# Performance work log

Hardware: AMD Instinct MI355X
Metric: run time of the kernel (lower is better)

The kernel has to match this reference:

```python
import jax, jax.numpy as jnp
import numpy as np

N_NODES = 50000
N_EDGES = 600000
D_IN = 128
D_HID = 128


def _gcn_layer(x, src, dst, W, b, n):
    # PyG GCNConv: h = x @ W; add self-loops; symmetric normalization
    # out_i = sum_j (d_i^-1/2 d_j^-1/2) h_j + (d_i^-1) h_i + b, with d = deg + 1
    h = x @ W  # [N, F]
    ones = jnp.ones(src.shape[0], dtype=x.dtype)
    deg = jax.ops.segment_sum(ones, dst, num_segments=n) + jnp.asarray(1.0, x.dtype)
    dinv = jax.lax.rsqrt(deg)  # [N]
    coef = dinv[src] * dinv[dst]  # [E]
    msg = h[src] * coef[:, None]  # gather + scale, [E, F]
    agg = jax.ops.segment_sum(msg, dst, num_segments=n)  # scatter-add, [N, F]
    agg = agg + h * (dinv * dinv)[:, None]  # self-loop contribution
    return agg + b


def setup_inputs() -> dict:
    key = jax.random.key(0)
    k1, k2, k3, k4 = jax.random.split(key, 4)
    x = jax.random.normal(k1, (N_NODES, D_IN), dtype=jnp.float32)
    edge_index = jax.random.randint(k2, (2, N_EDGES), 0, N_NODES, dtype=jnp.int32)
    # Glorot-ish init for linear weights
    W1 = jax.random.normal(k3, (D_IN, D_HID), dtype=jnp.float32) / np.sqrt(D_IN)
    W2 = jax.random.normal(k4, (D_HID, D_HID), dtype=jnp.float32) / np.sqrt(D_HID)
    b1 = jnp.zeros((D_HID,), dtype=jnp.float32)
    b2 = jnp.zeros((D_HID,), dtype=jnp.float32)
    return {"x": x, "edge_index": edge_index, "W1": W1, "b1": b1, "W2": W2, "b2": b2}


def reference(x, edge_index, W1, b1, W2, b2):
    src = edge_index[0]
    dst = edge_index[1]
    n = x.shape[0]
    h = _gcn_layer(x, src, dst, W1, b1, n)
    h = jax.nn.relu(h)
    out = _gcn_layer(h, src, dst, W2, b2, n)
    return out
```

## Files before the change

### kernel.cpp

```cpp
#include <hip/hip_runtime.h>
#include <hip/hip_bf16.h>

typedef __attribute__((ext_vector_type(8))) short short8;
typedef __attribute__((ext_vector_type(4))) float floatx4;

#define D 128
#define BCAP 2048
#define CPAD 16

__device__ __forceinline__ unsigned short f2bf(float f) {
    unsigned u = __float_as_uint(f);
    u += 0x7FFFu + ((u >> 16) & 1u);
    return (unsigned short)(u >> 16);
}
__device__ __forceinline__ float bf2f(unsigned short h) {
    return __uint_as_float(((unsigned)h) << 16);
}
__device__ __forceinline__ float bflo(unsigned p) { return __uint_as_float(p << 16); }
__device__ __forceinline__ float bfhi(unsigned p) { return __uint_as_float(p & 0xFFFF0000u); }

__global__ __launch_bounds__(256) void bucket_wconv_kernel(const int* __restrict__ src,
                                                           const int* __restrict__ dst,
                                                           int* __restrict__ bcnt,
                                                           unsigned* __restrict__ bucket, int E,
                                                           const float* __restrict__ W1,
                                                           const float* __restrict__ W2,
                                                           unsigned short* __restrict__ whi1,
                                                           unsigned short* __restrict__ wlo1,
                                                           unsigned short* __restrict__ whi2,
                                                           unsigned short* __restrict__ wlo2,
                                                           int eb4) {
    int b = blockIdx.x;
    if (b >= eb4) {
        int gid = (b - eb4) * 256 + threadIdx.x;
        int which = gid >> 14;
        int tid = gid & 16383;
        const float* W = which ? W2 : W1;
        unsigned short* whi = which ? whi2 : whi1;
        unsigned short* wlo = which ? wlo2 : wlo1;
        int j    = tid & 7;
        int col  = (tid >> 3) & 127;
        int quad = (tid >> 10) & 3;
        int kb   = tid >> 12;
        float wv = W[(kb * 32 + quad * 8 + j) * D + col];
        unsigned u = __float_as_uint(wv);
        unsigned short h = (unsigned short)(u >> 16);
        whi[tid] = h;
        wlo[tid] = f2bf(wv - bf2f(h));
        return;
    }
    int sub = b & 7;
    int t4 = (b * 256 + threadIdx.x) * 4;
    if (t4 + 3 < E) {
        int4 s = *reinterpret_cast<const int4*>(src + t4);
        int4 d = *reinterpret_cast<const int4*>(dst + t4);
        #pragma unroll
        for (int k = 0; k < 4; k++) {
            int dd = (k == 0) ? d.x : (k == 1) ? d.y : (k == 2) ? d.z : d.w;
            int ss = (k == 0) ? s.x : (k == 1) ? s.y : (k == 2) ? s.z : s.w;
            int slot = ((dd >> 8) << 3) | sub;
            int pos = atomicAdd(&bcnt[slot * CPAD], 1);
            if (pos < BCAP)
                bucket[(size_t)slot * BCAP + pos] = ((unsigned)(dd & 255) << 16) | (unsigned)ss;
        }
    } else {
        for (int i = t4; i < E; i++) {
            int dd = dst[i], ss = src[i];
            int slot = ((dd >> 8) << 3) | sub;
            int pos = atomicAdd(&bcnt[slot * CPAD], 1);
            if (pos < BCAP)
                bucket[(size_t)slot * BCAP + pos] = ((unsigned)(dd & 255) << 16) | (unsigned)ss;
        }
    }
}

__device__ __forceinline__ int block_excl_scan256(int v, int* lds, int tid) {
    int lane = tid & 63, wid = tid >> 6;
    int x = v;
    #pragma unroll
    for (int d = 1; d < 64; d <<= 1) {
        int y = __shfl_up(x, d, 64);
        if (lane >= d) x += y;
    }
    if (lane == 63) lds[wid] = x;
    __syncthreads();
    if (tid == 0) {
        int run = 0;
        #pragma unroll
        for (int i = 0; i < 4; i++) { int t2 = lds[i]; lds[i] = run; run += t2; }
    }
    __syncthreads();
    return lds[wid] + x - v;
}

__global__ __launch_bounds__(256) void build_gemm_kernel(const unsigned* __restrict__ bucket,
                                                         const int* __restrict__ bcnt,
                                                         int* __restrict__ row_ptr,
                                                         float* __restrict__ dinv,
                                                         int* __restrict__ esrc, int N, int E,
                                                         const float* __restrict__ A,
                                                         const unsigned short* __restrict__ whi,
                                                         const unsigned short* __restrict__ wlo,
                                                         unsigned short* __restrict__ C, int M,
                                                         int nbuk) {
    __shared__ int lds4[4];
    __shared__ int sbase[256];
    __shared__ int hist[256];
    __shared__ int cur[256];
    int tid = threadIdx.x;
    int b = blockIdx.x;
    if (b < nbuk) {
        int tot = 0;
        if (tid < nbuk) {
            #pragma unroll
            for (int s = 0; s < 8; s++) tot += min(bcnt[(tid * 8 + s) * CPAD], BCAP);
        }
        int ex = block_excl_scan256(tot, lds4, tid);
        sbase[tid] = ex;
        hist[tid] = 0;
        __syncthreads();
        int base = sbase[b];
        for (int sub = 0; sub < 8; sub++) {
            int cnt = min(bcnt[(b * 8 + sub) * CPAD], BCAP);
            const unsigned* bp = bucket + (size_t)(b * 8 + sub) * BCAP;
            for (int i = tid; i < cnt; i += 256)
                atomicAdd(&hist[bp[i] >> 16], 1);
        }
        __syncthreads();
        int h = hist[tid];
        int off = block_excl_scan256(h, lds4, tid);
        cur[tid] = base + off;
        int node = b * 256 + tid;
        if (node < N) {
            row_ptr[node] = base + off;
            dinv[node] = rsqrtf((float)(h + 1));
        }
        if (b == 0 && tid == 0) row_ptr[N] = E;
        __syncthreads();
        for (int sub = 0; sub < 8; sub++) {
            int cnt = min(bcnt[(b * 8 + sub) * CPAD], BCAP);
            const unsigned* bp = bucket + (size_t)(b * 8 + sub) * BCAP;
            for (int i = tid; i < cnt; i += 256) {
                unsigned v = bp[i];
                int p = atomicAdd(&cur[v >> 16], 1);
                esrc[p] = (int)(v & 0xFFFFu);
            }
        }
        return;
    }
    int lane = tid & 63, wid = tid >> 6;
    int quad = lane >> 4, l15 = lane & 15;
    int row0 = (b - nbuk) * 64;
    int n0 = wid * 32;

    short8 bhi[2][4], blo[2][4];
    #pragma unroll
    for (int t = 0; t < 2; t++)
        #pragma unroll
        for (int kb = 0; kb < 4; kb++) {
            size_t base = ((size_t)((kb * 4 + quad) * 128 + (n0 + t * 16 + l15))) * 8;
            bhi[t][kb] = *reinterpret_cast<const short8*>(whi + base);
            blo[t][kb] = *reinterpret_cast<const short8*>(wlo + base);
        }

    #pragma unroll
    for (int rg = 0; rg < 4; rg++) {
        int r0 = row0 + rg * 16;
        int ar = r0 + l15; if (ar > M - 1) ar = M - 1;
        short8 ahi[4], alo[4];
        #pragma unroll
        for (int kb = 0; kb < 4; kb++) {
            const float4* ap = reinterpret_cast<const float4*>(A + (size_t)ar * D + kb * 32 + quad * 8);
            float4 v0 = ap[0], v1 = ap[1];
            float vv[8] = {v0.x, v0.y, v0.z, v0.w, v1.x, v1.y, v1.z, v1.w};
            short8 vh, vl;
            #pragma unroll
            for (int j = 0; j < 8; j++) {
                unsigned u = __float_as_uint(vv[j]);
                unsigned short h = (unsigned short)(u >> 16);
                vh[j] = (short)h;
                vl[j] = (short)f2bf(vv[j] - bf2f(h));
            }
            ahi[kb] = vh;
            alo[kb] = vl;
        }
        floatx4 acc0 = {0.f, 0.f, 0.f, 0.f};
        floatx4 acc1 = {0.f, 0.f, 0.f, 0.f};
        #pragma unroll
        for (int kb = 0; kb < 4; kb++) {
            acc0 = __builtin_amdgcn_mfma_f32_16x16x32_bf16(ahi[kb], bhi[0][kb], acc0, 0, 0, 0);
            acc1 = __builtin_amdgcn_mfma_f32_16x16x32_bf16(ahi[kb], bhi[1][kb], acc1, 0, 0, 0);
            acc0 = __builtin_amdgcn_mfma_f32_16x16x32_bf16(ahi[kb], blo[0][kb], acc0, 0, 0, 0);
            acc1 = __builtin_amdgcn_mfma_f32_16x16x32_bf16(ahi[kb], blo[1][kb], acc1, 0, 0, 0);
            acc0 = __builtin_amdgcn_mfma_f32_16x16x32_bf16(alo[kb], bhi[0][kb], acc0, 0, 0, 0);
            acc1 = __builtin_amdgcn_mfma_f32_16x16x32_bf16(alo[kb], bhi[1][kb], acc1, 0, 0, 0);
        }
        #pragma unroll
        for (int r = 0; r < 4; r++) {
            int orow = r0 + quad * 4 + r;
            if (orow < M) {
                C[(size_t)orow * D + n0 + l15]      = f2bf(acc0[r]);
                C[(size_t)orow * D + n0 + 16 + l15] = f2bf(acc1[r]);
            }
        }
    }
}

__global__ __launch_bounds__(256) void gemm_bf16a_kernel(const unsigned short* __restrict__ A,
                                                         const unsigned short* __restrict__ whi,
                                                         const unsigned short* __restrict__ wlo,
                                                         unsigned short* __restrict__ C, int M) {
    int lane = threadIdx.x & 63, wid = threadIdx.x >> 6;
    int quad = lane >> 4, l15 = lane & 15;
    int row0 = blockIdx.x * 64;
    int n0 = wid * 32;

    short8 bhi[2][4], blo[2][4];
    #pragma unroll
    for (int t = 0; t < 2; t++)
        #pragma unroll
        for (int kb = 0; kb < 4; kb++) {
            size_t base = ((size_t)((kb * 4 + quad) * 128 + (n0 + t * 16 + l15))) * 8;
            bhi[t][kb] = *reinterpret_cast<const short8*>(whi + base);
            blo[t][kb] = *reinterpret_cast<const short8*>(wlo + base);
        }

    #pragma unroll
    for (int rg = 0; rg < 4; rg++) {
        int r0 = row0 + rg * 16;
        int ar = r0 + l15; if (ar > M - 1) ar = M - 1;
        short8 af[4];
        #pragma unroll
        for (int kb = 0; kb < 4; kb++)
            af[kb] = *reinterpret_cast<const short8*>(A + (size_t)ar * D + kb * 32 + quad * 8);
        floatx4 acc0 = {0.f, 0.f, 0.f, 0.f};
        floatx4 acc1 = {0.f, 0.f, 0.f, 0.f};
        #pragma unroll
        for (int kb = 0; kb < 4; kb++) {
            acc0 = __builtin_amdgcn_mfma_f32_16x16x32_bf16(af[kb], bhi[0][kb], acc0, 0, 0, 0);
            acc1 = __builtin_amdgcn_mfma_f32_16x16x32_bf16(af[kb], bhi[1][kb], acc1, 0, 0, 0);
            acc0 = __builtin_amdgcn_mfma_f32_16x16x32_bf16(af[kb], blo[0][kb], acc0, 0, 0, 0);
            acc1 = __builtin_amdgcn_mfma_f32_16x16x32_bf16(af[kb], blo[1][kb], acc1, 0, 0, 0);
        }
        #pragma unroll
        for (int r = 0; r < 4; r++) {
            int orow = r0 + quad * 4 + r;
            if (orow < M) {
                C[(size_t)orow * D + n0 + l15]      = f2bf(acc0[r]);
                C[(size_t)orow * D + n0 + 16 + l15] = f2bf(acc1[r]);
            }
        }
    }
}

__device__ __forceinline__ void agg_qbody(const uint4* __restrict__ H4,
                                          const float* __restrict__ dinv,
                                          const int* __restrict__ row_ptr,
                                          const int* __restrict__ esrc,
                                          const float* __restrict__ bias,
                                          int node, int fl, float* acc) {
    #pragma unroll
    for (int j = 0; j < 8; j++) acc[j] = 0.f;
    int beg = row_ptr[node], end = row_ptr[node + 1];
    int e = beg;
    for (; e + 4 <= end; e += 4) {
        int s0 = esrc[e], s1 = esrc[e + 1], s2 = esrc[e + 2], s3 = esrc[e + 3];
        float c0 = dinv[s0], c1 = dinv[s1], c2 = dinv[s2], c3 = dinv[s3];
        uint4 p0 = H4[(size_t)s0 * 16 + fl];
        uint4 p1 = H4[(size_t)s1 * 16 + fl];
        uint4 p2 = H4[(size_t)s2 * 16 + fl];
        uint4 p3 = H4[(size_t)s3 * 16 + fl];
        acc[0] += c0 * bflo(p0.x) + c1 * bflo(p1.x) + c2 * bflo(p2.x) + c3 * bflo(p3.x);
        acc[1] += c0 * bfhi(p0.x) + c1 * bfhi(p1.x) + c2 * bfhi(p2.x) + c3 * bfhi(p3.x);
        acc[2] += c0 * bflo(p0.y) + c1 * bflo(p1.y) + c2 * bflo(p2.y) + c3 * bflo(p3.y);
        acc[3] += c0 * bfhi(p0.y) + c1 * bfhi(p1.y) + c2 * bfhi(p2.y) + c3 * bfhi(p3.y);
        acc[4] += c0 * bflo(p0.z) + c1 * bflo(p1.z) + c2 * bflo(p2.z) + c3 * bflo(p3.z);
        acc[5] += c0 * bfhi(p0.z) + c1 * bfhi(p1.z) + c2 * bfhi(p2.z) + c3 * bfhi(p3.z);
        acc[6] += c0 * bflo(p0.w) + c1 * bflo(p1.w) + c2 * bflo(p2.w) + c3 * bflo(p3.w);
        acc[7] += c0 * bfhi(p0.w) + c1 * bfhi(p1.w) + c2 * bfhi(p2.w) + c3 * bfhi(p3.w);
    }
    for (; e < end; e++) {
        int s0 = esrc[e];
        float c = dinv[s0];
        uint4 p0 = H4[(size_t)s0 * 16 + fl];
        acc[0] += c * bflo(p0.x); acc[1] += c * bfhi(p0.x);
        acc[2] += c * bflo(p0.y); acc[3] += c * bfhi(p0.y);
        acc[4] += c * bflo(p0.z); acc[5] += c * bfhi(p0.z);
        acc[6] += c * bflo(p0.w); acc[7] += c * bfhi(p0.w);
    }
    float di = dinv[node];
    float dii = di * di;
    uint4 ps = H4[(size_t)node * 16 + fl];
    const float4* b4 = (const float4*)bias;
    float4 bb0 = b4[fl * 2], bb1 = b4[fl * 2 + 1];
    #pragma unroll
    for (int j = 0; j < 8; j++) acc[j] *= di;
    acc[0] += dii * bflo(ps.x) + bb0.x;
    acc[1] += dii * bfhi(ps.x) + bb0.y;
    acc[2] += dii * bflo(ps.y) + bb0.z;
    acc[3] += dii * bfhi(ps.y) + bb0.w;
    acc[4] += dii * bflo(ps.z) + bb1.x;
    acc[5] += dii * bfhi(ps.z) + bb1.y;
    acc[6] += dii * bflo(ps.w) + bb1.z;
    acc[7] += dii * bfhi(ps.w) + bb1.w;
}

__global__ __launch_bounds__(256) void agg_bf16out_kernel(const unsigned short* __restrict__ H,
                                                          const float* __restrict__ dinv,
                                                          const int* __restrict__ row_ptr,
                                                          const int* __restrict__ esrc,
                                                          const float* __restrict__ bias,
                                                          uint4* __restrict__ out, int N) {
    int node = blockIdx.x * 16 + (threadIdx.x >> 4);
    int fl = threadIdx.x & 15;
    if (node >= N) return;
    float acc[8];
    agg_qbody((const uint4*)H, dinv, row_ptr, esrc, bias, node, fl, acc);
    uint4 o;
    o.x = (unsigned)f2bf(fmaxf(acc[0], 0.f)) | ((unsigned)f2bf(fmaxf(acc[1], 0.f)) << 16);
    o.y = (unsigned)f2bf(fmaxf(acc[2], 0.f)) | ((unsigned)f2bf(fmaxf(acc[3], 0.f)) << 16);
    o.z = (unsigned)f2bf(fmaxf(acc[4], 0.f)) | ((unsigned)f2bf(fmaxf(acc[5], 0.f)) << 16);
    o.w = (unsigned)f2bf(fmaxf(acc[6], 0.f)) | ((unsigned)f2bf(fmaxf(acc[7], 0.f)) << 16);
    out[(size_t)node * 16 + fl] = o;
}

__global__ __launch_bounds__(256) void agg_f32out_kernel(const unsigned short* __restrict__ H,
                                                         const float* __restrict__ dinv,
                                                         const int* __restrict__ row_ptr,
                                                         const int* __restrict__ esrc,
                                                         const float* __restrict__ bias,
                                                         float4* __restrict__ out, int N) {
    int node = blockIdx.x * 16 + (threadIdx.x >> 4);
    int fl = threadIdx.x & 15;
    if (node >= N) return;
    float acc[8];
    agg_qbody((const uint4*)H, dinv, row_ptr, esrc, bias, node, fl, acc);
    float4 o0, o1;
    o0.x = acc[0]; o0.y = acc[1]; o0.z = acc[2]; o0.w = acc[3];
    o1.x = acc[4]; o1.y = acc[5]; o1.z = acc[6]; o1.w = acc[7];
    out[(size_t)node * 32 + fl * 2]     = o0;
    out[(size_t)node * 32 + fl * 2 + 1] = o1;
}

extern "C" void kernel_launch(void* const* d_in, const int* in_sizes, int n_in,
                              void* d_out, int out_size, void* d_ws, size_t ws_size,
                              hipStream_t stream) {
    const float* x  = (const float*)d_in[0];
    const int*   ei = (const int*)d_in[1];
    const float* W1 = (const float*)d_in[2];
    const float* b1 = (const float*)d_in[3];
    const float* W2 = (const float*)d_in[4];
    const float* b2 = (const float*)d_in[5];

    int N = in_sizes[0] / D;
    int E = in_sizes[1] / 2;
    const int* src = ei;
    const int* dst = ei + E;

    int nbuk = (N + 255) / 256;

    char* ws = (char*)d_ws;
    int*      bcnt   = (int*)(ws + 0);
    unsigned* bucket = (unsigned*)(ws + 102400);
    int*      row_ptr= (int*)(ws + 12947456);
    float*    dinv   = (float*)(ws + 13147520);
    int*      esrcs  = (int*)(ws + 13347520);
    unsigned short* whi1 = (unsigned short*)(ws + 15747584);
    unsigned short* wlo1 = (unsigned short*)(ws + 15780352);
    unsigned short* whi2 = (unsigned short*)(ws + 15813120);
    unsigned short* wlo2 = (unsigned short*)(ws + 15845888);
    unsigned short* hfeat = (unsigned short*)(ws + 15878656);
    unsigned short* hmid  = (unsigned short*)(ws + 28678656);

    int eb4  = (E / 4 + 255) / 256;
    int gb   = (N + 63) / 64;
    int ab16 = (N + 15) / 16;

    hipMemsetAsync(bcnt, 0, (size_t)nbuk * 8 * CPAD * sizeof(int), stream);
    bucket_wconv_kernel<<<eb4 + 128, 256, 0, stream>>>(src, dst, bcnt, bucket, E,
                                                       W1, W2, whi1, wlo1, whi2, wlo2, eb4);

    build_gemm_kernel<<<nbuk + gb, 256, 0, stream>>>(bucket, bcnt, row_ptr, dinv, esrcs,
                                                     N, E, x, whi1, wlo1, hfeat, N, nbuk);

    agg_bf16out_kernel<<<ab16, 256, 0, stream>>>(hfeat, dinv, row_ptr, esrcs, b1,
                                                 (uint4*)hmid, N);

    gemm_bf16a_kernel<<<gb, 256, 0, stream>>>(hmid, whi2, wlo2, hfeat, N);
    agg_f32out_kernel<<<ab16, 256, 0, stream>>>(hfeat, dinv, row_ptr, esrcs, b2,
                                                (float4*)d_out, N);
}
```

Measured before the change: 204.0 us.

## Fuse layer-1 aggregation with layer-2 GEMM via shared-memory tile

The first-layer aggregation kernel now keeps each block's 16 aggregated, ReLU'd bf16 rows in shared memory and multiplies them straight by W2 with MFMA. This replaces the separate aggregation kernel and second GEMM kernel, removing one launch and the global write and read of the intermediate hidden matrix. In exchange, each 16-row block reloads the W2 hi/lo fragments from global or cache memory, adds a block-wide barrier, and does a small GEMM tile per block, which may underuse the matrix units.

```diff
diff --git a/kernel.cpp b/kernel.cpp
--- a/kernel.cpp
+++ b/kernel.cpp
@@ -206,53 +206,6 @@
     }
 }
 
-__global__ __launch_bounds__(256) void gemm_bf16a_kernel(const unsigned short* __restrict__ A,
-                                                         const unsigned short* __restrict__ whi,
-                                                         const unsigned short* __restrict__ wlo,
-                                                         unsigned short* __restrict__ C, int M) {
-    int lane = threadIdx.x & 63, wid = threadIdx.x >> 6;
-    int quad = lane >> 4, l15 = lane & 15;
-    int row0 = blockIdx.x * 64;
-    int n0 = wid * 32;
-
-    short8 bhi[2][4], blo[2][4];
-    #pragma unroll
-    for (int t = 0; t < 2; t++)
-        #pragma unroll
-        for (int kb = 0; kb < 4; kb++) {
-            size_t base = ((size_t)((kb * 4 + quad) * 128 + (n0 + t * 16 + l15))) * 8;
-            bhi[t][kb] = *reinterpret_cast<const short8*>(whi + base);
-            blo[t][kb] = *reinterpret_cast<const short8*>(wlo + base);
-        }
-
-    #pragma unroll
-    for (int rg = 0; rg < 4; rg++) {
-        int r0 = row0 + rg * 16;
-        int ar = r0 + l15; if (ar > M - 1) ar = M - 1;
-        short8 af[4];
-        #pragma unroll
-        for (int kb = 0; kb < 4; kb++)
-            af[kb] = *reinterpret_cast<const short8*>(A + (size_t)ar * D + kb * 32 + quad * 8);
-        floatx4 acc0 = {0.f, 0.f, 0.f, 0.f};
-        floatx4 acc1 = {0.f, 0.f, 0.f, 0.f};
-        #pragma unroll
-        for (int kb = 0; kb < 4; kb++) {
-            acc0 = __builtin_amdgcn_mfma_f32_16x16x32_bf16(af[kb], bhi[0][kb], acc0, 0, 0, 0);
-            acc1 = __builtin_amdgcn_mfma_f32_16x16x32_bf16(af[kb], bhi[1][kb], acc1, 0, 0, 0);
-            acc0 = __builtin_amdgcn_mfma_f32_16x16x32_bf16(af[kb], blo[0][kb], acc0, 0, 0, 0);
-            acc1 = __builtin_amdgcn_mfma_f32_16x16x32_bf16(af[kb], blo[1][kb], acc1, 0, 0, 0);
-        }
-        #pragma unroll
-        for (int r = 0; r < 4; r++) {
-            int orow = r0 + quad * 4 + r;
-            if (orow < M) {
-                C[(size_t)orow * D + n0 + l15]      = f2bf(acc0[r]);
-                C[(size_t)orow * D + n0 + 16 + l15] = f2bf(acc1[r]);
-            }
-        }
-    }
-}
-
 __device__ __forceinline__ void agg_qbody(const uint4* __restrict__ H4,
                                           const float* __restrict__ dinv,
                                           const int* __restrict__ row_ptr,
@@ -305,23 +258,59 @@
     acc[7] += dii * bfhi(ps.w) + bb1.w;
 }
 
-__global__ __launch_bounds__(256) void agg_bf16out_kernel(const unsigned short* __restrict__ H,
-                                                          const float* __restrict__ dinv,
-                                                          const int* __restrict__ row_ptr,
-                                                          const int* __restrict__ esrc,
-                                                          const float* __restrict__ bias,
-                                                          uint4* __restrict__ out, int N) {
-    int node = blockIdx.x * 16 + (threadIdx.x >> 4);
-    int fl = threadIdx.x & 15;
-    if (node >= N) return;
+__global__ __launch_bounds__(256) void agg_gemm2_kernel(const unsigned short* __restrict__ H,
+                                                        const float* __restrict__ dinv,
+                                                        const int* __restrict__ row_ptr,
+                                                        const int* __restrict__ esrc,
+                                                        const float* __restrict__ bias,
+                                                        const unsigned short* __restrict__ whi,
+                                                        const unsigned short* __restrict__ wlo,
+                                                        unsigned short* __restrict__ C, int N) {
+    __shared__ unsigned short Asm[16 * 136];
+    int tid = threadIdx.x;
+    int node0 = blockIdx.x * 16;
+    int r = tid >> 4;
+    int fl = tid & 15;
+    int node = node0 + r;
     float acc[8];
-    agg_qbody((const uint4*)H, dinv, row_ptr, esrc, bias, node, fl, acc);
-    uint4 o;
-    o.x = (unsigned)f2bf(fmaxf(acc[0], 0.f)) | ((unsigned)f2bf(fmaxf(acc[1], 0.f)) << 16);
-    o.y = (unsigned)f2bf(fmaxf(acc[2], 0.f)) | ((unsigned)f2bf(fmaxf(acc[3], 0.f)) << 16);
-    o.z = (unsigned)f2bf(fmaxf(acc[4], 0.f)) | ((unsigned)f2bf(fmaxf(acc[5], 0.f)) << 16);
-    o.w = (unsigned)f2bf(fmaxf(acc[6], 0.f)) | ((unsigned)f2bf(fmaxf(acc[7], 0.f)) << 16);
-    out[(size_t)node * 16 + fl] = o;
+    if (node < N) {
+        agg_qbody((const uint4*)H, dinv, row_ptr, esrc, bias, node, fl, acc);
+    } else {
+        #pragma unroll
+        for (int j = 0; j < 8; j++) acc[j] = 0.f;
+    }
+    short8 a;
+    #pragma unroll
+    for (int j = 0; j < 8; j++) a[j] = (short)f2bf(fmaxf(acc[j], 0.f));
+    *reinterpret_cast<short8*>(&Asm[r * 136 + fl * 8]) = a;
+    __syncthreads();
+
+    int lane = tid & 63, wid = tid >> 6;
+    int quad = lane >> 4, l15 = lane & 15;
+    int n0 = wid * 32;
+    floatx4 acc0 = {0.f, 0.f, 0.f, 0.f};
+    floatx4 acc1 = {0.f, 0.f, 0.f, 0.f};
+    #pragma unroll 1
+    for (int kb = 0; kb < 4; kb++) {
+        size_t wb = ((size_t)((kb * 4 + quad) * 128 + (n0 + l15))) * 8;
+        short8 bh0 = *reinterpret_cast<const short8*>(whi + wb);
+        short8 bh1 = *reinterpret_cast<const short8*>(whi + wb + 128);
+        short8 bl0 = *reinterpret_cast<const short8*>(wlo + wb);
+        short8 bl1 = *reinterpret_cast<const short8*>(wlo + wb + 128);
+        short8 af = *reinterpret_cast<const short8*>(&Asm[l15 * 136 + kb * 32 + quad * 8]);
+        acc0 = __builtin_amdgcn_mfma_f32_16x16x32_bf16(af, bh0, acc0, 0, 0, 0);
+        acc1 = __builtin_amdgcn_mfma_f32_16x16x32_bf16(af, bh1, acc1, 0, 0, 0);
+        acc0 = __builtin_amdgcn_mfma_f32_16x16x32_bf16(af, bl0, acc0, 0, 0, 0);
+        acc1 = __builtin_amdgcn_mfma_f32_16x16x32_bf16(af, bl1, acc1, 0, 0, 0);
+    }
+    #pragma unroll
+    for (int rr = 0; rr < 4; rr++) {
+        int orow = node0 + quad * 4 + rr;
+        if (orow < N) {
+            C[(size_t)orow * D + n0 + l15]      = f2bf(acc0[rr]);
+            C[(size_t)orow * D + n0 + 16 + l15] = f2bf(acc1[rr]);
+        }
+    }
 }
 
 __global__ __launch_bounds__(256) void agg_f32out_kernel(const unsigned short* __restrict__ H,
@@ -370,7 +359,7 @@
     unsigned short* whi2 = (unsigned short*)(ws + 15813120);
     unsigned short* wlo2 = (unsigned short*)(ws + 15845888);
     unsigned short* hfeat = (unsigned short*)(ws + 15878656);
-    unsigned short* hmid  = (unsigned short*)(ws + 28678656);
+    unsigned short* h2    = (unsigned short*)(ws + 28678656);
 
     int eb4  = (E / 4 + 255) / 256;
     int gb   = (N + 63) / 64;
@@ -383,10 +372,9 @@
     build_gemm_kernel<<<nbuk + gb, 256, 0, stream>>>(bucket, bcnt, row_ptr, dinv, esrcs,
                                                      N, E, x, whi1, wlo1, hfeat, N, nbuk);
 
-    agg_bf16out_kernel<<<ab16, 256, 0, stream>>>(hfeat, dinv, row_ptr, esrcs, b1,
-                                                 (uint4*)hmid, N);
-
-    gemm_bf16a_kernel<<<gb, 256, 0, stream>>>(hmid, whi2, wlo2, hfeat, N);
-    agg_f32out_kernel<<<ab16, 256, 0, stream>>>(hfeat, dinv, row_ptr, esrcs, b2,
+    agg_gemm2_kernel<<<ab16, 256, 0, stream>>>(hfeat, dinv, row_ptr, esrcs, b1,
+                                               whi2, wlo2, h2, N);
+
+    agg_f32out_kernel<<<ab16, 256, 0, stream>>>(h2, dinv, row_ptr, esrcs, b2,
                                                 (float4*)d_out, N);
 }
```

After: 192.4 us. 1.06x faster.
